# Optimization experiments

Measured on AMD Instinct MI355X. Metric: run time of the kernel, lower is better.

The kernel has to match this reference:

```python
import jax, jax.numpy as jnp
import numpy as np

IN_BIT = 8      # in_bit_width
W_BIT = 2       # weight_bit_width (also output act quantizer bit width)
BN_EPS = 1e-4


def _ste(x, q):
    # straight-through estimator: forward = q, backward = identity w.r.t. x
    return x + jax.lax.stop_gradient(q - x)


def act_quant(x, bit):
    # CommonActQuant: signed int quant, narrow_range=False, power-of-two scale
    # range [-1, 1 - 2^{-(bit-1)}] -> scale = 2^{-(bit-1)}
    s = 2.0 ** (1 - bit)
    n_min = -(2.0 ** (bit - 1))
    n_max = 2.0 ** (bit - 1) - 1.0
    q = jnp.clip(jnp.round(x / s), n_min, n_max) * s
    return _ste(x, q)


def weight_quant(w, bit):
    # CommonWeightQuant: narrow-range signed int quant, unit scaling const
    # scale = 1 / (2^{bit-1} - 1); for bit=2 levels are {-1, 0, 1}
    n = 2.0 ** (bit - 1) - 1.0
    s = 1.0 / n
    q = jnp.clip(jnp.round(w / s), -n, n) * s
    return _ste(w, q)


def setup_inputs() -> dict:
    key = jax.random.key(0)
    k1, k2, k3, k4 = jax.random.split(key, 4)
    B, C, H, W = 32, 256, 32, 32
    x = jax.random.normal(k1, (B, C, H, W), dtype=jnp.float32) * 0.5
    weight = jax.random.normal(k2, (C, C, 3, 3), dtype=jnp.float32) * 0.5
    gamma = jnp.ones((C,), dtype=jnp.float32)
    beta = jnp.zeros((C,), dtype=jnp.float32)
    running_mean = jax.random.normal(k3, (C,), dtype=jnp.float32) * 0.1
    running_var = jax.random.uniform(k4, (C,), dtype=jnp.float32, minval=0.5, maxval=1.5)
    return {"x": x, "weight": weight, "gamma": gamma, "beta": beta,
            "running_mean": running_mean, "running_var": running_var}


def reference(x, weight, gamma, beta, running_mean, running_var):
    # 1) input QuantIdentity (8-bit, [-1, 1-2^-7], power-of-two scale 2^-7)
    xq = act_quant(x, IN_BIT)
    # 2) QuantConv2d 3x3 stride 1 pad 1, no bias, 2-bit weights
    wq = weight_quant(weight, W_BIT)
    y = jax.lax.conv_general_dilated(
        xq, wq, window_strides=(1, 1), padding=((1, 1), (1, 1)),
        dimension_numbers=("NCHW", "OIHW", "NCHW"))
    # 3) BatchNorm2d (inference, eps=1e-4)
    inv = gamma / jnp.sqrt(running_var + BN_EPS)
    y = y * inv[None, :, None, None] + (beta - running_mean * inv)[None, :, None, None]
    # 4) output QuantIdentity at weight_bit_width bits
    return act_quant(y, W_BIT)
```

## Files before the change

### kernel.cpp

```cpp
#include <hip/hip_runtime.h>
#include <hip/hip_bf16.h>
#include <stdint.h>


typedef int i32x4 __attribute__((ext_vector_type(4)));
typedef float f32x4 __attribute__((ext_vector_type(4)));

__device__ __forceinline__ void gload_lds16(const void* g, const void* lds) {
    __builtin_amdgcn_global_load_lds(
        (const __attribute__((address_space(1))) unsigned int*)(uintptr_t)g,
        (__attribute__((address_space(3))) unsigned int*)(uintptr_t)lds,
        16, 0, 0);
}

__global__ __launch_bounds__(256) void quant_kernel(
    const float* __restrict__ x, const float* __restrict__ w,
    signed char* __restrict__ xpad, signed char* __restrict__ wq)
{
    __shared__ signed char tile[32 * 272];
    const int t = threadIdx.x;
    const int blk = blockIdx.x;

    if (blk >= 1088) {
        const int co = blk - 1088;
        signed char* wt = tile;
#pragma unroll
        for (int p = 0; p < 9; ++p) {
            const int idx = p * 256 + t;
            const float v = w[co * 2304 + idx];
            const int ci = idx / 9;
            const int khkw = idx - 9 * ci;
            const float q = fminf(fmaxf(rintf(v), -1.f), 1.f);
            wt[khkw * 256 + ci] = (signed char)(int)q;
        }
        __syncthreads();
        if (t < 144) {
            const int kt = t >> 2, kq = t & 3;
            const uint4 v = *(const uint4*)(wt + t * 16);
            *(uint4*)(wq + ((size_t)((co >> 4) * 36 + kt) << 10) + kq * 256 + (co & 15) * 16) = v;
        }
        return;
    }

    const int b = blk / 34;
    const int hp = blk % 34;
    signed char* rowbase = xpad + (size_t)((b * 34 + hp) * 34) * 256;
    const uint4 z = {0u, 0u, 0u, 0u};
    if (hp == 0 || hp == 33) {
        for (int i = t; i < 544; i += 256) *(uint4*)(rowbase + i * 16) = z;
        return;
    }
    const int h = hp - 1;
    const float* xb = x + ((size_t)(b * 256) * 32 + h) * 32;

#pragma unroll
    for (int q2 = 0; q2 < 2; ++q2) {
        const int beta = q2 * 256 + t;
        const int cib = beta >> 3;
        const int w4 = beta & 7;
        unsigned row[4];
#pragma unroll
        for (int j = 0; j < 4; ++j) {
            const f32x4 v = *(const f32x4*)(xb + (size_t)(cib * 4 + j) * 1024 + w4 * 4);
            unsigned p = 0;
#pragma unroll
            for (int k = 0; k < 4; ++k) {
                const float q = fminf(fmaxf(rintf(__fmul_rn(v[k], 128.f)), -128.f), 127.f);
                p |= ((unsigned)(unsigned char)(signed char)(int)q) << (8 * k);
            }
            row[j] = p;
        }
        const unsigned ab_lo = __builtin_amdgcn_perm(row[1], row[0], 0x05010400u);
        const unsigned ab_hi = __builtin_amdgcn_perm(row[1], row[0], 0x07030602u);
        const unsigned cd_lo = __builtin_amdgcn_perm(row[3], row[2], 0x05010400u);
        const unsigned cd_hi = __builtin_amdgcn_perm(row[3], row[2], 0x07030602u);
        unsigned col[4];
        col[0] = __builtin_amdgcn_perm(cd_lo, ab_lo, 0x05040100u);
        col[1] = __builtin_amdgcn_perm(cd_lo, ab_lo, 0x07060302u);
        col[2] = __builtin_amdgcn_perm(cd_hi, ab_hi, 0x05040100u);
        col[3] = __builtin_amdgcn_perm(cd_hi, ab_hi, 0x07060302u);
#pragma unroll
        for (int r = 0; r < 4; ++r)
            *(unsigned*)(tile + (w4 * 4 + r) * 272 + cib * 4) = col[r];
    }
    __syncthreads();
#pragma unroll
    for (int q = 0; q < 2; ++q) {
        const int wp = q * 16 + (t >> 4);
        const int ci16 = (t & 15) * 16;
        uint4 v = *(const uint4*)(tile + wp * 272 + ci16);
        *(uint4*)(rowbase + (size_t)(wp + 1) * 256 + ci16) = v;
    }
    if (t < 32) {
        const int wp = (t >> 4) * 33;
        *(uint4*)(rowbase + (size_t)wp * 256 + (t & 15) * 16) = z;
    }
}

__global__ __launch_bounds__(512, 4) void conv_gemm_kernel(
    const signed char* __restrict__ xpad, const signed char* __restrict__ wqm,
    const float* __restrict__ gamma, const float* __restrict__ beta,
    const float* __restrict__ mean, const float* __restrict__ var,
    float* __restrict__ out)
{
    __shared__ signed char As[6 * 34 * 256];

    const int tid = threadIdx.x;
    const int wv = tid >> 6;
    const int lane = tid & 63;
    const int l16 = lane & 15;
    const int l4 = lane >> 4;

    const int bid = (int)blockIdx.x;
    const int swz = (bid & 7) * 64 + (bid >> 3);

    const int mt = swz >> 1;
    const int n0 = (swz & 1) * 128;
    const int b = mt >> 3;
    const int h0 = (mt & 7) * 4;
    const int wave_m = wv & 1;
    const int wave_n = wv >> 1;

    const signed char* xbase = xpad + (size_t)(b * 34 + h0) * 34 * 256;
#pragma unroll
    for (int p = 0; p < 7; ++p) {
        const int i = p * 8 + wv;
        if (i < 51) {
            const int d = i * 64 + lane;
            const int r = d >> 4;
            const int c = d & 15;
            gload_lds16(xbase + r * 256 + ((c ^ (r & 15)) << 4), As + i * 1024);
        }
    }
    __syncthreads();

    int r0[4];
#pragma unroll
    for (int i = 0; i < 4; ++i)
        r0[i] = (wave_m * 2 + (i >> 1)) * 34 + (i & 1) * 16 + l16;

    const signed char* bp0 = wqm + (((size_t)((n0 >> 4) + wave_n * 2 + 0) * 36) << 10) + lane * 16;
    const signed char* bp1 = wqm + (((size_t)((n0 >> 4) + wave_n * 2 + 1) * 36) << 10) + lane * 16;

    i32x4 acc[4][2];
#pragma unroll
    for (int i = 0; i < 4; i++)
#pragma unroll
        for (int j = 0; j < 2; j++) acc[i][j] = (i32x4){0, 0, 0, 0};

    i32x4 aP[2][4], bP[3][2];

#define LOAD_B(kt, dst) { dst[0] = *(const i32x4*)(bp0 + (kt) * 1024); \
                          dst[1] = *(const i32x4*)(bp1 + (kt) * 1024); }
#define LOAD_A(kt, dst) { const int khkw = (kt) >> 2; \
                          const int kh = khkw / 3; \
                          const int kw = khkw - 3 * kh; \
                          const int roff = kh * 34 + kw; \
                          const int cb = ((kt) & 3) * 4 + l4; \
                          _Pragma("unroll") \
                          for (int i = 0; i < 4; ++i) { \
                              const int r = r0[i] + roff; \
                              dst[i] = *(const i32x4*)(As + r * 256 + ((cb ^ (r & 15)) << 4)); \
                          } }
#define MFMA(af, bf) { _Pragma("unroll") \
                       for (int i = 0; i < 4; ++i) \
                           _Pragma("unroll") \
                           for (int j = 0; j < 2; ++j) \
                               acc[i][j] = __builtin_amdgcn_mfma_i32_16x16x64_i8(af[i], bf[j], acc[i][j], 0, 0, 0); }

    LOAD_B(0, bP[0])
    LOAD_B(1, bP[1])
    LOAD_A(0, aP[0])
#pragma unroll
    for (int kt = 0; kt < 36; ++kt) {
        if (kt + 2 < 36) { LOAD_B(kt + 2, bP[(kt + 2) % 3]) }
        if (kt + 1 < 36) { LOAD_A(kt + 1, aP[(kt + 1) & 1]) }
        MFMA(aP[kt & 1], bP[kt % 3])
    }

#pragma unroll
    for (int j = 0; j < 2; ++j) {
        const int co = n0 + wave_n * 32 + j * 16 + l16;
        const float iv = __fdiv_rn(gamma[co], __fsqrt_rn(__fadd_rn(var[co], 1e-4f)));
        const float bias = __fsub_rn(beta[co], __fmul_rn(mean[co], iv));
#pragma unroll
        for (int i = 0; i < 4; ++i) {
            const int h = h0 + wave_m * 2 + (i >> 1);
            const int w = (i & 1) * 16 + l4 * 4;
            f32x4 v;
#pragma unroll
            for (int r = 0; r < 4; r++) {
                const float y = __fmul_rn((float)acc[i][j][r], 0.0078125f);
                const float t = __fadd_rn(__fmul_rn(y, iv), bias);
                float z = rintf(__fmul_rn(t, 2.f));
                z = fminf(fmaxf(z, -2.f), 1.f);
                v[r] = __fmul_rn(z, 0.5f);
            }
            *(f32x4*)(&out[(((size_t)(b * 256 + co)) * 32 + h) * 32 + w]) = v;
        }
    }
#undef LOAD_B
#undef LOAD_A
#undef MFMA
}

extern "C" void kernel_launch(void* const* d_in, const int* in_sizes, int n_in,
                              void* d_out, int out_size, void* d_ws, size_t ws_size,
                              hipStream_t stream) {
    const float* x      = (const float*)d_in[0];
    const float* weight = (const float*)d_in[1];
    const float* gamma  = (const float*)d_in[2];
    const float* beta   = (const float*)d_in[3];
    const float* rmean  = (const float*)d_in[4];
    const float* rvar   = (const float*)d_in[5];
    float* out = (float*)d_out;

    signed char* wq   = (signed char*)d_ws;
    signed char* xpad = (signed char*)d_ws + (1 << 20);

    quant_kernel<<<1344, 256, 0, stream>>>(x, weight, xpad, wq);
    conv_gemm_kernel<<<512, 512, 0, stream>>>(xpad, wq, gamma, beta, rmean, rvar, out);
}
```

Measured before the change: 113.3 us.

## Fuse input activation quantization into conv GEMM prologue, drop padded int8 buffer

```diff
diff --git a/kernel.cpp b/kernel.cpp
--- a/kernel.cpp
+++ b/kernel.cpp
@@ -6,99 +6,31 @@
 typedef int i32x4 __attribute__((ext_vector_type(4)));
 typedef float f32x4 __attribute__((ext_vector_type(4)));
 
-__device__ __forceinline__ void gload_lds16(const void* g, const void* lds) {
-    __builtin_amdgcn_global_load_lds(
-        (const __attribute__((address_space(1))) unsigned int*)(uintptr_t)g,
-        (__attribute__((address_space(3))) unsigned int*)(uintptr_t)lds,
-        16, 0, 0);
+__global__ __launch_bounds__(256) void wquant_kernel(
+    const float* __restrict__ w, signed char* __restrict__ wq)
+{
+    __shared__ signed char wt[9 * 256];
+    const int t = threadIdx.x;
+    const int co = blockIdx.x;
+#pragma unroll
+    for (int p = 0; p < 9; ++p) {
+        const int idx = p * 256 + t;
+        const float v = w[co * 2304 + idx];
+        const int ci = idx / 9;
+        const int khkw = idx - 9 * ci;
+        const float q = fminf(fmaxf(rintf(v), -1.f), 1.f);
+        wt[khkw * 256 + ci] = (signed char)(int)q;
+    }
+    __syncthreads();
+    if (t < 144) {
+        const int kt = t >> 2, kq = t & 3;
+        const uint4 v = *(const uint4*)(wt + t * 16);
+        *(uint4*)(wq + ((size_t)((co >> 4) * 36 + kt) << 10) + kq * 256 + (co & 15) * 16) = v;
+    }
 }
 
-__global__ __launch_bounds__(256) void quant_kernel(
-    const float* __restrict__ x, const float* __restrict__ w,
-    signed char* __restrict__ xpad, signed char* __restrict__ wq)
-{
-    __shared__ signed char tile[32 * 272];
-    const int t = threadIdx.x;
-    const int blk = blockIdx.x;
-
-    if (blk >= 1088) {
-        const int co = blk - 1088;
-        signed char* wt = tile;
-#pragma unroll
-        for (int p = 0; p < 9; ++p) {
-            const int idx = p * 256 + t;
-            const float v = w[co * 2304 + idx];
-            const int ci = idx / 9;
-            const int khkw = idx - 9 * ci;
-            const float q = fminf(fmaxf(rintf(v), -1.f), 1.f);
-            wt[khkw * 256 + ci] = (signed char)(int)q;
-        }
-        __syncthreads();
-        if (t < 144) {
-            const int kt = t >> 2, kq = t & 3;
-            const uint4 v = *(const uint4*)(wt + t * 16);
-            *(uint4*)(wq + ((size_t)((co >> 4) * 36 + kt) << 10) + kq * 256 + (co & 15) * 16) = v;
-        }
-        return;
-    }
-
-    const int b = blk / 34;
-    const int hp = blk % 34;
-    signed char* rowbase = xpad + (size_t)((b * 34 + hp) * 34) * 256;
-    const uint4 z = {0u, 0u, 0u, 0u};
-    if (hp == 0 || hp == 33) {
-        for (int i = t; i < 544; i += 256) *(uint4*)(rowbase + i * 16) = z;
-        return;
-    }
-    const int h = hp - 1;
-    const float* xb = x + ((size_t)(b * 256) * 32 + h) * 32;
-
-#pragma unroll
-    for (int q2 = 0; q2 < 2; ++q2) {
-        const int beta = q2 * 256 + t;
-        const int cib = beta >> 3;
-        const int w4 = beta & 7;
-        unsigned row[4];
-#pragma unroll
-        for (int j = 0; j < 4; ++j) {
-            const f32x4 v = *(const f32x4*)(xb + (size_t)(cib * 4 + j) * 1024 + w4 * 4);
-            unsigned p = 0;
-#pragma unroll
-            for (int k = 0; k < 4; ++k) {
-                const float q = fminf(fmaxf(rintf(__fmul_rn(v[k], 128.f)), -128.f), 127.f);
-                p |= ((unsigned)(unsigned char)(signed char)(int)q) << (8 * k);
-            }
-            row[j] = p;
-        }
-        const unsigned ab_lo = __builtin_amdgcn_perm(row[1], row[0], 0x05010400u);
-        const unsigned ab_hi = __builtin_amdgcn_perm(row[1], row[0], 0x07030602u);
-        const unsigned cd_lo = __builtin_amdgcn_perm(row[3], row[2], 0x05010400u);
-        const unsigned cd_hi = __builtin_amdgcn_perm(row[3], row[2], 0x07030602u);
-        unsigned col[4];
-        col[0] = __builtin_amdgcn_perm(cd_lo, ab_lo, 0x05040100u);
-        col[1] = __builtin_amdgcn_perm(cd_lo, ab_lo, 0x07060302u);
-        col[2] = __builtin_amdgcn_perm(cd_hi, ab_hi, 0x05040100u);
-        col[3] = __builtin_amdgcn_perm(cd_hi, ab_hi, 0x07060302u);
-#pragma unroll
-        for (int r = 0; r < 4; ++r)
-            *(unsigned*)(tile + (w4 * 4 + r) * 272 + cib * 4) = col[r];
-    }
-    __syncthreads();
-#pragma unroll
-    for (int q = 0; q < 2; ++q) {
-        const int wp = q * 16 + (t >> 4);
-        const int ci16 = (t & 15) * 16;
-        uint4 v = *(const uint4*)(tile + wp * 272 + ci16);
-        *(uint4*)(rowbase + (size_t)(wp + 1) * 256 + ci16) = v;
-    }
-    if (t < 32) {
-        const int wp = (t >> 4) * 33;
-        *(uint4*)(rowbase + (size_t)wp * 256 + (t & 15) * 16) = z;
-    }
-}
-
 __global__ __launch_bounds__(512, 4) void conv_gemm_kernel(
-    const signed char* __restrict__ xpad, const signed char* __restrict__ wqm,
+    const float* __restrict__ x, const signed char* __restrict__ wqm,
     const float* __restrict__ gamma, const float* __restrict__ beta,
     const float* __restrict__ mean, const float* __restrict__ var,
     float* __restrict__ out)
@@ -121,32 +53,8 @@
     const int wave_m = wv & 1;
     const int wave_n = wv >> 1;
 
-    const signed char* xbase = xpad + (size_t)(b * 34 + h0) * 34 * 256;
-#pragma unroll
-    for (int p = 0; p < 7; ++p) {
-        const int i = p * 8 + wv;
-        if (i < 51) {
-            const int d = i * 64 + lane;
-            const int r = d >> 4;
-            const int c = d & 15;
-            gload_lds16(xbase + r * 256 + ((c ^ (r & 15)) << 4), As + i * 1024);
-        }
-    }
-    __syncthreads();
-
-    int r0[4];
-#pragma unroll
-    for (int i = 0; i < 4; ++i)
-        r0[i] = (wave_m * 2 + (i >> 1)) * 34 + (i & 1) * 16 + l16;
-
     const signed char* bp0 = wqm + (((size_t)((n0 >> 4) + wave_n * 2 + 0) * 36) << 10) + lane * 16;
     const signed char* bp1 = wqm + (((size_t)((n0 >> 4) + wave_n * 2 + 1) * 36) << 10) + lane * 16;
-
-    i32x4 acc[4][2];
-#pragma unroll
-    for (int i = 0; i < 4; i++)
-#pragma unroll
-        for (int j = 0; j < 2; j++) acc[i][j] = (i32x4){0, 0, 0, 0};
 
     i32x4 aP[2][4], bP[3][2];
 
@@ -170,6 +78,81 @@
 
     LOAD_B(0, bP[0])
     LOAD_B(1, bP[1])
+
+    const uint4 z = {0u, 0u, 0u, 0u};
+    if (tid < 192) {
+        const int pair = tid >> 4;
+        const int hh = pair >> 1;
+        const int wp = (pair & 1) * 33;
+        const bool covered = (h0 == 0 && hh == 0) || (h0 == 28 && hh == 5);
+        if (!covered) {
+            const int r = hh * 34 + wp;
+            const int ch = tid & 15;
+            *(uint4*)(As + r * 256 + ((ch ^ (r & 15)) << 4)) = z;
+        }
+    }
+    if (h0 == 0) {
+        for (int i = tid; i < 544; i += 512) {
+            const int r = i >> 4;
+            const int ch = i & 15;
+            *(uint4*)(As + r * 256 + ((ch ^ (r & 15)) << 4)) = z;
+        }
+    }
+    if (h0 == 28) {
+        for (int i = tid; i < 544; i += 512) {
+            const int r = 5 * 34 + (i >> 4);
+            const int ch = i & 15;
+            *(uint4*)(As + r * 256 + ((ch ^ (r & 15)) << 4)) = z;
+        }
+    }
+
+    const int cib = tid >> 3;
+    const int w4 = tid & 7;
+#pragma unroll
+    for (int hh = 0; hh < 6; ++hh) {
+        const int h = h0 + hh - 1;
+        if (h < 0 || h > 31) continue;
+        const float* xb = x + ((size_t)(b * 256) * 32 + h) * 32;
+        unsigned row[4];
+#pragma unroll
+        for (int j = 0; j < 4; ++j) {
+            const f32x4 v = *(const f32x4*)(xb + (size_t)(cib * 4 + j) * 1024 + w4 * 4);
+            unsigned p = 0;
+#pragma unroll
+            for (int k = 0; k < 4; ++k) {
+                const float q = fminf(fmaxf(rintf(__fmul_rn(v[k], 128.f)), -128.f), 127.f);
+                p |= ((unsigned)(unsigned char)(signed char)(int)q) << (8 * k);
+            }
+            row[j] = p;
+        }
+        const unsigned ab_lo = __builtin_amdgcn_perm(row[1], row[0], 0x05010400u);
+        const unsigned ab_hi = __builtin_amdgcn_perm(row[1], row[0], 0x07030602u);
+        const unsigned cd_lo = __builtin_amdgcn_perm(row[3], row[2], 0x05010400u);
+        const unsigned cd_hi = __builtin_amdgcn_perm(row[3], row[2], 0x07030602u);
+        unsigned col[4];
+        col[0] = __builtin_amdgcn_perm(cd_lo, ab_lo, 0x05040100u);
+        col[1] = __builtin_amdgcn_perm(cd_lo, ab_lo, 0x07060302u);
+        col[2] = __builtin_amdgcn_perm(cd_hi, ab_hi, 0x05040100u);
+        col[3] = __builtin_amdgcn_perm(cd_hi, ab_hi, 0x07060302u);
+#pragma unroll
+        for (int r = 0; r < 4; ++r) {
+            const int rr = hh * 34 + w4 * 4 + r + 1;
+            *(unsigned*)(As + rr * 256 + (((cib >> 2) ^ (rr & 15)) << 4) + (cib & 3) * 4) = col[r];
+        }
+    }
+    __syncthreads();
+
+    int r0[4];
+#pragma unroll
+    for (int i = 0; i < 4; ++i)
+        r0[i] = (wave_m * 2 + (i >> 1)) * 34 + (i & 1) * 16 + l16;
+
+    i32x4 acc[4][2];
+#pragma unroll
+    for (int i = 0; i < 4; i++)
+#pragma unroll
+        for (int j = 0; j < 2; j++) acc[i][j] = (i32x4){0, 0, 0, 0};
+
     LOAD_A(0, aP[0])
 #pragma unroll
     for (int kt = 0; kt < 36; ++kt) {
@@ -192,9 +175,9 @@
             for (int r = 0; r < 4; r++) {
                 const float y = __fmul_rn((float)acc[i][j][r], 0.0078125f);
                 const float t = __fadd_rn(__fmul_rn(y, iv), bias);
-                float z = rintf(__fmul_rn(t, 2.f));
-                z = fminf(fmaxf(z, -2.f), 1.f);
-                v[r] = __fmul_rn(z, 0.5f);
+                float z2 = rintf(__fmul_rn(t, 2.f));
+                z2 = fminf(fmaxf(z2, -2.f), 1.f);
+                v[r] = __fmul_rn(z2, 0.5f);
             }
             *(f32x4*)(&out[(((size_t)(b * 256 + co)) * 32 + h) * 32 + w]) = v;
         }
@@ -215,9 +198,8 @@
     const float* rvar   = (const float*)d_in[5];
     float* out = (float*)d_out;
 
-    signed char* wq   = (signed char*)d_ws;
-    signed char* xpad = (signed char*)d_ws + (1 << 20);
-
-    quant_kernel<<<1344, 256, 0, stream>>>(x, weight, xpad, wq);
-    conv_gemm_kernel<<<512, 512, 0, stream>>>(xpad, wq, gamma, beta, rmean, rvar, out);
+    signed char* wq = (signed char*)d_ws;
+
+    wquant_kernel<<<256, 256, 0, stream>>>(weight, wq);
+    conv_gemm_kernel<<<512, 512, 0, stream>>>(x, wq, gamma, beta, rmean, rvar, out);
 }
```

After: 113.6 us. Within noise of the previous version (+0.2%).
